# Optimization experiments

Measured on AMD Instinct MI355X. Metric: run time of the kernel, lower is better.

## Reference

```python
import jax, jax.numpy as jnp
import numpy as np

E = 1_000_000   # edges (temporal neighbor facts)
D = 128         # emb_dim
N = 200_000     # nodes carrying hidden state
B = 512         # queries (batch)
R = 240         # num_rel -> rel table has 2R+1 rows
T = 100_000     # tail nodes (scatter output size)


def setup_inputs() -> dict:
    key = jax.random.key(0)
    ks = jax.random.split(key, 14)
    b_col  = jax.random.randint(ks[0], (E,), 0, B)
    n_col  = jax.random.randint(ks[1], (E,), 0, N)
    h_col  = jax.random.randint(ks[2], (E,), 0, N)
    r_col  = jax.random.randint(ks[3], (E,), 0, 2 * R)   # r+1 in [1, 2R]
    t_col  = jax.random.randint(ks[4], (E,), 0, N)
    ts_col = jax.random.randint(ks[5], (E,), 0, 1000)
    facts = jnp.stack([b_col, n_col, h_col, r_col, t_col, ts_col], axis=1)
    s = 1.0 / np.sqrt(D)
    return {
        "hidden":     jax.random.normal(ks[6], (N, D), jnp.float32) * 0.02,
        "rel_table":  jax.random.normal(ks[7], (2 * R + 1, D), jnp.float32) * 0.02,
        "Ws":         jax.random.normal(ks[8], (D, D), jnp.float32) * s,
        "Wr":         jax.random.normal(ks[9], (D, D), jnp.float32) * s,
        "Wqr_w":      jax.random.normal(ks[10], (D, D), jnp.float32) * s,
        "Wqr_b":      jnp.zeros((D,), jnp.float32),
        "wa_w":       jax.random.normal(ks[11], (D, 1), jnp.float32) * s,
        "wa_b":       jnp.zeros((1,), jnp.float32),
        "Wh":         jax.random.normal(ks[12], (D, D), jnp.float32) * s,
        "query_rel":  jax.random.randint(ks[13], (B,), 0, 2 * R),
        "facts":      facts,
        "tail_index": jax.random.randint(jax.random.fold_in(key, 99), (E,), 0, T),
        "tail_nodes": jnp.arange(T),
    }


def reference(hidden, rel_table, Ws, Wr, Wqr_w, Wqr_b, wa_w, wa_b, Wh,
              query_rel, facts, tail_index, tail_nodes):
    b = facts[:, 0]
    n = facts[:, 1]
    r = facts[:, 3]
    h_e = hidden[n]                      # [E, D] gather node hidden
    hr  = rel_table[r + 1]               # [E, D] gather relation emb
    q_r = rel_table[query_rel + 1][b]    # [E, D] per-edge query relation
    # attention MLP: sigmoid(w_alpha(relu(Ws h + Wr r + Wqr q + b)))
    pre = h_e @ Ws + hr @ Wr + (q_r @ Wqr_w + Wqr_b)          # [E, D]
    alpha = jax.nn.sigmoid(jax.nn.relu(pre) @ wa_w + wa_b)    # [E, 1]
    message = alpha * (h_e + hr)                              # [E, D]
    agg = jax.ops.segment_sum(message, tail_index,
                              num_segments=tail_nodes.shape[0])  # [T, D]
    return agg @ Wh                      # act = identity (default)
```

## Files before the change

### kernel.cpp

```cpp
#include <hip/hip_runtime.h>
#include <hip/hip_fp16.h>
#include <math.h>

#define DD 128
#define CAP 64

typedef _Float16 half_t;
typedef __attribute__((ext_vector_type(8))) _Float16 half8;
typedef __attribute__((ext_vector_type(4))) float floatx4;

#define LDW 136

__device__ __forceinline__ __half2 relu2(__half2 x) {
    return __hmul2(x, __hgt2(x, __float2half2_rn(0.f)));
}

template <int CTRL>
__device__ __forceinline__ float dpp_add(float x) {
    int y = __builtin_amdgcn_update_dpp(0, __float_as_int(x), CTRL, 0xf, 0xf, true);
    return x + __int_as_float(y);
}

__global__ void wt4(const float* __restrict__ W0, const float* __restrict__ W1,
                    const float* __restrict__ W2, const float* __restrict__ W3,
                    half_t* __restrict__ T0, half_t* __restrict__ T1,
                    half_t* __restrict__ T2, half_t* __restrict__ T3) {
    const float* W = blockIdx.x == 0 ? W0 : blockIdx.x == 1 ? W1 : blockIdx.x == 2 ? W2 : W3;
    half_t* T      = blockIdx.x == 0 ? T0 : blockIdx.x == 1 ? T1 : blockIdx.x == 2 ? T2 : T3;
    for (int i = threadIdx.x; i < DD * DD; i += blockDim.x) {
        int n = i >> 7, k = i & 127;
        T[i] = (half_t)W[(size_t)k * DD + n];
    }
}

__device__ __forceinline__ void mfma_pass(
    const half_t* As, const half_t* WT, int w, int lane, floatx4 acc[8]) {
    int rowf = lane & 15;
    int kgrp = (lane >> 4) * 8;
#pragma unroll
    for (int t = 0; t < 8; t++) acc[t] = (floatx4){0.f, 0.f, 0.f, 0.f};
    const half_t* ap = As + (w * 16 + rowf) * LDW + kgrp;
    const half_t* bp0 = WT + rowf * LDW + kgrp;
#pragma unroll
    for (int kk = 0; kk < DD; kk += 32) {
        half8 a = *(const half8*)(ap + kk);
#pragma unroll
        for (int t = 0; t < 8; t++) {
            half8 b = *(const half8*)(bp0 + t * 16 * LDW + kk);
            acc[t] = __builtin_amdgcn_mfma_f32_16x16x32_f16(a, b, acc[t], 0, 0, 0);
        }
    }
}

__device__ __forceinline__ void acc_to_lds(const floatx4 acc[8], half_t* OutT,
                                           int w, int lane) {
    int rowf = lane & 15;
    int rbase = w * 16 + (lane >> 4) * 4;
#pragma unroll
    for (int t = 0; t < 8; t++) {
        int col = t * 16 + rowf;
#pragma unroll
        for (int i = 0; i < 4; i++) OutT[(rbase + i) * LDW + col] = (half_t)acc[t][i];
    }
}

__device__ __forceinline__ void lds_to_packed(const half_t* OutT, int tileM, int M,
                                              int tid, __half* Packed, int halfOff) {
    for (int ch = tid; ch < 1024; ch += 256) {
        int row = ch >> 4, off = (ch & 15) * 8;
        int gr = tileM + row;
        if (gr < M) {
            half8 v = *(const half8*)(OutT + row * LDW + off);
            *(uint4*)(Packed + (size_t)gr * 256 + halfOff + off) = *(uint4*)&v;
        }
    }
}

__global__ __launch_bounds__(256) void gemm_pack2(
    const float* __restrict__ table, int M,
    const half_t* __restrict__ WT1_g, const half_t* __restrict__ WT2_g,
    __half* __restrict__ Packed) {
    __shared__ half_t WT[DD * LDW];
    __shared__ half_t As[64 * LDW];
    int tid = threadIdx.x;
    int lane = tid & 63;
    int w = tid >> 6;
    int tileM = blockIdx.x * 64;

    for (int i = tid; i < 2048; i += 256) {
        int row = i >> 5, c4 = i & 31;
        int gr = tileM + row;
        float4 v = make_float4(0.f, 0.f, 0.f, 0.f);
        if (gr < M) v = *(const float4*)(table + (size_t)gr * DD + c4 * 4);
        __half2 h01 = __floats2half2_rn(v.x, v.y);
        __half2 h23 = __floats2half2_rn(v.z, v.w);
        *(uint2*)(As + row * LDW + c4 * 4) = make_uint2(*(unsigned*)&h01, *(unsigned*)&h23);
    }
    for (int i = tid; i < 2048; i += 256) {
        int n = i >> 4, ch = i & 15;
        *(half8*)(WT + n * LDW + ch * 8) = *(const half8*)(WT1_g + n * DD + ch * 8);
    }
    __syncthreads();
    floatx4 acc[8];
    mfma_pass(As, WT, w, lane, acc);
    __syncthreads();
    acc_to_lds(acc, WT, w, lane);
    __syncthreads();
    lds_to_packed(WT, tileM, M, tid, Packed, 0);
    __syncthreads();
    for (int i = tid; i < 2048; i += 256) {
        int n = i >> 4, ch = i & 15;
        *(half8*)(WT + n * LDW + ch * 8) = *(const half8*)(WT2_g + n * DD + ch * 8);
    }
    __syncthreads();
    mfma_pass(As, WT, w, lane, acc);
    __syncthreads();
    acc_to_lds(acc, WT, w, lane);
    __syncthreads();
    lds_to_packed(WT, tileM, M, tid, Packed, 128);
}

__global__ __launch_bounds__(256) void gemm_mfma(
    const float* __restrict__ table, const int* __restrict__ idx, int idxAdd, int M,
    const half_t* __restrict__ WT_g, const float* __restrict__ bias,
    float* __restrict__ OutF, __half* __restrict__ OutH) {
    __shared__ half_t WT[DD * LDW];
    __shared__ half_t As[64 * LDW];
    int tid = threadIdx.x;
    int lane = tid & 63;
    int w = tid >> 6;
    int rowf = lane & 15;

    for (int i = tid; i < 2048; i += 256) {
        int n = i >> 4, ch = i & 15;
        *(half8*)(WT + n * LDW + ch * 8) = *(const half8*)(WT_g + n * DD + ch * 8);
    }
    int tileM = blockIdx.x * 64;
    for (int i = tid; i < 2048; i += 256) {
        int row = i >> 5, c4 = i & 31;
        int gr = tileM + row;
        float4 v = make_float4(0.f, 0.f, 0.f, 0.f);
        if (gr < M) {
            int src = idx ? (idx[gr] + idxAdd) : gr;
            v = *(const float4*)(table + (size_t)src * DD + c4 * 4);
        }
        __half2 h01 = __floats2half2_rn(v.x, v.y);
        __half2 h23 = __floats2half2_rn(v.z, v.w);
        *(uint2*)(As + row * LDW + c4 * 4) = make_uint2(*(unsigned*)&h01, *(unsigned*)&h23);
    }
    __syncthreads();

    floatx4 acc[8];
    mfma_pass(As, WT, w, lane, acc);
    int orow = tileM + w * 16 + (lane >> 4) * 4;
#pragma unroll
    for (int t = 0; t < 8; t++) {
        int col = t * 16 + rowf;
        float bv = bias ? bias[col] : 0.f;
#pragma unroll
        for (int i = 0; i < 4; i++) {
            int gr = orow + i;
            if (gr < M) {
                float o = acc[t][i] + bv;
                if (OutF) OutF[(size_t)gr * DD + col] = o;
                if (OutH) OutH[(size_t)gr * DD + col] = __float2half(o);
            }
        }
    }
}

__global__ __launch_bounds__(256) void alpha_scatter(
    const __half* __restrict__ HB, const __half* __restrict__ RB,
    const __half* __restrict__ QB, const int* __restrict__ facts,
    const int* __restrict__ tail, const float* __restrict__ wa,
    const float* __restrict__ wa_b,
    int* __restrict__ cursor, int2* __restrict__ meta, int E) {
    int tid = threadIdx.x;
    int lane = tid & 63;
    int g = lane >> 4;
    int cl = lane & 15;
    int c = cl * 8;
    int wv = (blockIdx.x * 256 + tid) >> 6;
    int e0 = wv * 16 + g;

    float4 wva = *(const float4*)(wa + c);
    float4 wvb = *(const float4*)(wa + c + 4);
    __half2 w0 = __halves2half2(__float2half(wva.x), __float2half(wva.y));
    __half2 w1 = __halves2half2(__float2half(wva.z), __float2half(wva.w));
    __half2 w2 = __halves2half2(__float2half(wvb.x), __float2half(wvb.y));
    __half2 w3 = __halves2half2(__float2half(wvb.z), __float2half(wvb.w));
    float wb = wa_b[0];

    bool v[4]; int2 bn[4]; int r[4]; int tl[4];
#pragma unroll
    for (int j = 0; j < 4; j++) {
        int f = e0 + j * 4;
        v[j] = f < E;
        int fc = v[j] ? f : 0;
        bn[j] = *(const int2*)(facts + (size_t)fc * 6);
        r[j] = facts[(size_t)fc * 6 + 3];
        tl[j] = tail[fc];
    }

    uint4 h[4], rr[4], q[4];
#pragma unroll
    for (int j = 0; j < 4; j++) {
        h[j]  = *(const uint4*)(HB + (size_t)bn[j].y * 256 + 128 + c);
        rr[j] = *(const uint4*)(RB + (size_t)(r[j] + 1) * 256 + 128 + c);
        q[j]  = *(const uint4*)(QB + (size_t)bn[j].x * DD + c);
    }

    float t[4];
#pragma unroll
    for (int j = 0; j < 4; j++) {
        __half2 p0 = relu2(__hadd2(__hadd2(*(__half2*)&h[j].x, *(__half2*)&rr[j].x),
                                   *(__half2*)&q[j].x));
        __half2 p1 = relu2(__hadd2(__hadd2(*(__half2*)&h[j].y, *(__half2*)&rr[j].y),
                                   *(__half2*)&q[j].y));
        __half2 p2 = relu2(__hadd2(__hadd2(*(__half2*)&h[j].z, *(__half2*)&rr[j].z),
                                   *(__half2*)&q[j].z));
        __half2 p3 = relu2(__hadd2(__hadd2(*(__half2*)&h[j].w, *(__half2*)&rr[j].w),
                                   *(__half2*)&q[j].w));
        __half2 t2 = __hfma2(p1, w1, __hmul2(p0, w0));
        t2 = __hfma2(p2, w2, t2);
        t2 = __hfma2(p3, w3, t2);
        t[j] = __half2float(__low2half(t2)) + __half2float(__high2half(t2));
    }

#pragma unroll
    for (int j = 0; j < 4; j++) {
        t[j] = dpp_add<0x111>(t[j]);
        t[j] = dpp_add<0x112>(t[j]);
        t[j] = dpp_add<0x114>(t[j]);
        t[j] = dpp_add<0x118>(t[j]);
    }

    if (cl == 15) {
#pragma unroll
        for (int j = 0; j < 4; j++) {
            if (v[j]) {
                float a = 1.f / (1.f + __expf(-(t[j] + wb)));
                unsigned ab = (unsigned)__half_as_ushort(__float2half(a));
                int slot = atomicAdd(&cursor[tl[j]], 1);
                if (slot < CAP)
                    meta[(size_t)tl[j] * CAP + slot] =
                        make_int2(bn[j].y, (r[j] + 1) | (int)(ab << 16));
            }
        }
    }
}

__global__ __launch_bounds__(256) void agg_out(
    const __half* __restrict__ HB, const __half* __restrict__ RB,
    const int2* __restrict__ meta, const int* __restrict__ cursor,
    float* __restrict__ out, int T) {
    int w = threadIdx.x >> 6;
    int lane = threadIdx.x & 63;
    int seg = blockIdx.x * 4 + w;
    if (seg >= T) return;
    int cnt = cursor[seg];
    if (cnt > CAP) cnt = CAP;
    const int2* mp = meta + (size_t)seg * CAP;
    int co = lane * 2;
    float ax = 0.f, ay = 0.f;

#define ACC(hu, ru, y_)                                                        \
    {                                                                          \
        __half2 s = __hadd2(*(__half2*)&(hu), *(__half2*)&(ru));               \
        float al =                                                             \
            __half2float(__ushort_as_half((unsigned short)((unsigned)(y_) >> 16))); \
        float2 sf = __half22float2(s);                                         \
        ax = fmaf(al, sf.x, ax);                                               \
        ay = fmaf(al, sf.y, ay);                                               \
    }

    int i = 0;
    for (; i + 7 < cnt; i += 8) {
        int4 ma = *(const int4*)(mp + i);
        int4 mb = *(const int4*)(mp + i + 2);
        int4 mc = *(const int4*)(mp + i + 4);
        int4 md = *(const int4*)(mp + i + 6);
        unsigned h0 = *(const unsigned*)(HB + (size_t)ma.x * 256 + co);
        unsigned r0 = *(const unsigned*)(RB + (size_t)(ma.y & 0xFFFF) * 256 + co);
        unsigned h1 = *(const unsigned*)(HB + (size_t)ma.z * 256 + co);
        unsigned r1 = *(const unsigned*)(RB + (size_t)(ma.w & 0xFFFF) * 256 + co);
        unsigned h2 = *(const unsigned*)(HB + (size_t)mb.x * 256 + co);
        unsigned r2 = *(const unsigned*)(RB + (size_t)(mb.y & 0xFFFF) * 256 + co);
        unsigned h3 = *(const unsigned*)(HB + (size_t)mb.z * 256 + co);
        unsigned r3 = *(const unsigned*)(RB + (size_t)(mb.w & 0xFFFF) * 256 + co);
        unsigned h4 = *(const unsigned*)(HB + (size_t)mc.x * 256 + co);
        unsigned r4 = *(const unsigned*)(RB + (size_t)(mc.y & 0xFFFF) * 256 + co);
        unsigned h5 = *(const unsigned*)(HB + (size_t)mc.z * 256 + co);
        unsigned r5 = *(const unsigned*)(RB + (size_t)(mc.w & 0xFFFF) * 256 + co);
        unsigned h6 = *(const unsigned*)(HB + (size_t)md.x * 256 + co);
        unsigned r6 = *(const unsigned*)(RB + (size_t)(md.y & 0xFFFF) * 256 + co);
        unsigned h7 = *(const unsigned*)(HB + (size_t)md.z * 256 + co);
        unsigned r7 = *(const unsigned*)(RB + (size_t)(md.w & 0xFFFF) * 256 + co);
        ACC(h0, r0, ma.y); ACC(h1, r1, ma.w);
        ACC(h2, r2, mb.y); ACC(h3, r3, mb.w);
        ACC(h4, r4, mc.y); ACC(h5, r5, mc.w);
        ACC(h6, r6, md.y); ACC(h7, r7, md.w);
    }
    for (; i + 3 < cnt; i += 4) {
        int4 ma = *(const int4*)(mp + i);
        int4 mb = *(const int4*)(mp + i + 2);
        unsigned h0 = *(const unsigned*)(HB + (size_t)ma.x * 256 + co);
        unsigned r0 = *(const unsigned*)(RB + (size_t)(ma.y & 0xFFFF) * 256 + co);
        unsigned h1 = *(const unsigned*)(HB + (size_t)ma.z * 256 + co);
        unsigned r1 = *(const unsigned*)(RB + (size_t)(ma.w & 0xFFFF) * 256 + co);
        unsigned h2 = *(const unsigned*)(HB + (size_t)mb.x * 256 + co);
        unsigned r2 = *(const unsigned*)(RB + (size_t)(mb.y & 0xFFFF) * 256 + co);
        unsigned h3 = *(const unsigned*)(HB + (size_t)mb.z * 256 + co);
        unsigned r3 = *(const unsigned*)(RB + (size_t)(mb.w & 0xFFFF) * 256 + co);
        ACC(h0, r0, ma.y); ACC(h1, r1, ma.w);
        ACC(h2, r2, mb.y); ACC(h3, r3, mb.w);
    }
    for (; i < cnt; i++) {
        int2 m = mp[i];
        unsigned hu = *(const unsigned*)(HB + (size_t)m.x * 256 + co);
        unsigned ru = *(const unsigned*)(RB + (size_t)(m.y & 0xFFFF) * 256 + co);
        ACC(hu, ru, m.y);
    }
#undef ACC

    *(float2*)(out + (size_t)seg * DD + co) = make_float2(ax, ay);
}

extern "C" void kernel_launch(void* const* d_in, const int* in_sizes, int n_in,
                              void* d_out, int out_size, void* d_ws, size_t ws_size,
                              hipStream_t stream) {
    const float* hidden    = (const float*)d_in[0];
    const float* rel_table = (const float*)d_in[1];
    const float* Ws        = (const float*)d_in[2];
    const float* Wr        = (const float*)d_in[3];
    const float* Wqr_w     = (const float*)d_in[4];
    const float* Wqr_b     = (const float*)d_in[5];
    const float* wa_w      = (const float*)d_in[6];
    const float* wa_b      = (const float*)d_in[7];
    const float* Wh        = (const float*)d_in[8];
    const int* query_rel   = (const int*)d_in[9];
    const int* facts       = (const int*)d_in[10];
    const int* tail_index  = (const int*)d_in[11];

    int N     = in_sizes[0] / DD;
    int Rrows = in_sizes[1] / DD;
    int B     = in_sizes[9];
    int E     = in_sizes[11];
    int T     = in_sizes[12];

    char* ws = (char*)d_ws;
    size_t off = 0;
    auto alloc = [&](size_t bytes) -> void* {
        void* p = ws + off;
        off += (bytes + 255) & ~(size_t)255;
        return p;
    };
    __half* HB  = (__half*)alloc((size_t)N * 256 * 2);
    __half* RB  = (__half*)alloc((size_t)Rrows * 256 * 2);
    __half* QB  = (__half*)alloc((size_t)B * DD * 2);
    int* cursor = (int*)alloc((size_t)T * 4);
    int2* meta  = (int2*)alloc((size_t)T * CAP * 8);
    half_t* WsT  = (half_t*)alloc((size_t)DD * DD * 2);
    half_t* WrT  = (half_t*)alloc((size_t)DD * DD * 2);
    half_t* WqrT = (half_t*)alloc((size_t)DD * DD * 2);
    half_t* WhT  = (half_t*)alloc((size_t)DD * DD * 2);

    (void)hipMemsetAsync(cursor, 0, (size_t)T * 4, stream);

    wt4<<<4, 256, 0, stream>>>(Ws, Wr, Wqr_w, Wh, WsT, WrT, WqrT, WhT);

    gemm_pack2<<<(N + 63) / 64, 256, 0, stream>>>(hidden, N, WhT, WsT, HB);
    gemm_pack2<<<(Rrows + 63) / 64, 256, 0, stream>>>(rel_table, Rrows, WhT, WrT, RB);
    gemm_mfma<<<(B + 63) / 64, 256, 0, stream>>>(rel_table, query_rel, 1, B,
                                                 WqrT, Wqr_b, nullptr, QB);

    alpha_scatter<<<(E + 63) / 64, 256, 0, stream>>>(HB, RB, QB, facts, tail_index,
                                                     wa_w, wa_b, cursor, meta, E);

    agg_out<<<(T + 3) / 4, 256, 0, stream>>>(HB, RB, meta, cursor,
                                             (float*)d_out, T);
}
```

Before: 448.2 us.

## Pre-swizzle weights into MFMA fragment order and stream A fragments from global

Weights are converted once into a layout that matches the MFMA B-fragment order, so each lane reads its fragment with one contiguous vector load. The node/relation projection kernel now uses 1024-thread blocks, each wave owning 16-row tiles. It loads A fragments straight from global memory into registers and writes results directly to global instead of going through LDS with several barriers. The cost is more LDS per block (two weight matrices), uncoalesced scalar half stores to the packed output, and lower occupancy from the larger block.

```diff
diff --git a/kernel.cpp b/kernel.cpp
--- a/kernel.cpp
+++ b/kernel.cpp
@@ -21,103 +21,89 @@
     return x + __int_as_float(y);
 }
 
-__global__ void wt4(const float* __restrict__ W0, const float* __restrict__ W1,
-                    const float* __restrict__ W2, const float* __restrict__ W3,
-                    half_t* __restrict__ T0, half_t* __restrict__ T1,
-                    half_t* __restrict__ T2, half_t* __restrict__ T3) {
-    const float* W = blockIdx.x == 0 ? W0 : blockIdx.x == 1 ? W1 : blockIdx.x == 2 ? W2 : W3;
-    half_t* T      = blockIdx.x == 0 ? T0 : blockIdx.x == 1 ? T1 : blockIdx.x == 2 ? T2 : T3;
-    for (int i = threadIdx.x; i < DD * DD; i += blockDim.x) {
-        int n = i >> 7, k = i & 127;
-        T[i] = (half_t)W[(size_t)k * DD + n];
-    }
-}
-
-__device__ __forceinline__ void mfma_pass(
-    const half_t* As, const half_t* WT, int w, int lane, floatx4 acc[8]) {
-    int rowf = lane & 15;
-    int kgrp = (lane >> 4) * 8;
-#pragma unroll
-    for (int t = 0; t < 8; t++) acc[t] = (floatx4){0.f, 0.f, 0.f, 0.f};
-    const half_t* ap = As + (w * 16 + rowf) * LDW + kgrp;
-    const half_t* bp0 = WT + rowf * LDW + kgrp;
-#pragma unroll
-    for (int kk = 0; kk < DD; kk += 32) {
-        half8 a = *(const half8*)(ap + kk);
-#pragma unroll
-        for (int t = 0; t < 8; t++) {
-            half8 b = *(const half8*)(bp0 + t * 16 * LDW + kk);
-            acc[t] = __builtin_amdgcn_mfma_f32_16x16x32_f16(a, b, acc[t], 0, 0, 0);
-        }
-    }
-}
-
-__device__ __forceinline__ void acc_to_lds(const floatx4 acc[8], half_t* OutT,
-                                           int w, int lane) {
-    int rowf = lane & 15;
-    int rbase = w * 16 + (lane >> 4) * 4;
-#pragma unroll
-    for (int t = 0; t < 8; t++) {
-        int col = t * 16 + rowf;
-#pragma unroll
-        for (int i = 0; i < 4; i++) OutT[(rbase + i) * LDW + col] = (half_t)acc[t][i];
-    }
-}
-
-__device__ __forceinline__ void lds_to_packed(const half_t* OutT, int tileM, int M,
-                                              int tid, __half* Packed, int halfOff) {
-    for (int ch = tid; ch < 1024; ch += 256) {
-        int row = ch >> 4, off = (ch & 15) * 8;
-        int gr = tileM + row;
-        if (gr < M) {
-            half8 v = *(const half8*)(OutT + row * LDW + off);
-            *(uint4*)(Packed + (size_t)gr * 256 + halfOff + off) = *(uint4*)&v;
-        }
-    }
-}
-
-__global__ __launch_bounds__(256) void gemm_pack2(
+__global__ void wprep(const float* __restrict__ Wh, const float* __restrict__ Ws,
+                      const float* __restrict__ Wr, const float* __restrict__ Wqr,
+                      half_t* __restrict__ WhF, half_t* __restrict__ WsF,
+                      half_t* __restrict__ WrF, half_t* __restrict__ WqrT) {
+    int m = blockIdx.x;
+    if (m < 3) {
+        const float* W = m == 0 ? Wh : m == 1 ? Ws : Wr;
+        half_t* F      = m == 0 ? WhF : m == 1 ? WsF : WrF;
+        for (int idx = threadIdx.x; idx < 2048; idx += blockDim.x) {
+            int lane = idx & 63, kkI = (idx >> 6) & 3, t = idx >> 8;
+            int n = t * 16 + (lane & 15);
+            int k0 = kkI * 32 + (lane >> 4) * 8;
+            half_t tmp[8];
+#pragma unroll
+            for (int j = 0; j < 8; j++) tmp[j] = (half_t)W[(size_t)(k0 + j) * DD + n];
+            *(half8*)(F + (size_t)idx * 8) = *(half8*)tmp;
+        }
+    } else {
+        for (int i = threadIdx.x; i < DD * DD; i += blockDim.x) {
+            int n = i >> 7, k = i & 127;
+            WqrT[i] = (half_t)Wqr[(size_t)k * DD + n];
+        }
+    }
+}
+
+__global__ __launch_bounds__(1024) void gemm_pack2v(
     const float* __restrict__ table, int M,
-    const half_t* __restrict__ WT1_g, const half_t* __restrict__ WT2_g,
+    const half_t* __restrict__ W1F, const half_t* __restrict__ W2F,
     __half* __restrict__ Packed) {
-    __shared__ half_t WT[DD * LDW];
-    __shared__ half_t As[64 * LDW];
+    __shared__ half_t WF[2 * 2048 * 8];
     int tid = threadIdx.x;
-    int lane = tid & 63;
-    int w = tid >> 6;
-    int tileM = blockIdx.x * 64;
-
-    for (int i = tid; i < 2048; i += 256) {
-        int row = i >> 5, c4 = i & 31;
-        int gr = tileM + row;
-        float4 v = make_float4(0.f, 0.f, 0.f, 0.f);
-        if (gr < M) v = *(const float4*)(table + (size_t)gr * DD + c4 * 4);
-        __half2 h01 = __floats2half2_rn(v.x, v.y);
-        __half2 h23 = __floats2half2_rn(v.z, v.w);
-        *(uint2*)(As + row * LDW + c4 * 4) = make_uint2(*(unsigned*)&h01, *(unsigned*)&h23);
-    }
-    for (int i = tid; i < 2048; i += 256) {
-        int n = i >> 4, ch = i & 15;
-        *(half8*)(WT + n * LDW + ch * 8) = *(const half8*)(WT1_g + n * DD + ch * 8);
+    for (int i = tid; i < 4096; i += 1024) {
+        const half_t* src = (i < 2048) ? (W1F + (size_t)i * 8)
+                                       : (W2F + (size_t)(i - 2048) * 8);
+        *(half8*)(WF + (size_t)i * 8) = *(const half8*)src;
     }
     __syncthreads();
-    floatx4 acc[8];
-    mfma_pass(As, WT, w, lane, acc);
-    __syncthreads();
-    acc_to_lds(acc, WT, w, lane);
-    __syncthreads();
-    lds_to_packed(WT, tileM, M, tid, Packed, 0);
-    __syncthreads();
-    for (int i = tid; i < 2048; i += 256) {
-        int n = i >> 4, ch = i & 15;
-        *(half8*)(WT + n * LDW + ch * 8) = *(const half8*)(WT2_g + n * DD + ch * 8);
-    }
-    __syncthreads();
-    mfma_pass(As, WT, w, lane, acc);
-    __syncthreads();
-    acc_to_lds(acc, WT, w, lane);
-    __syncthreads();
-    lds_to_packed(WT, tileM, M, tid, Packed, 128);
+
+    int w = tid >> 6, lane = tid & 63;
+    int nt = (M + 15) >> 4;
+    for (int tile = blockIdx.x * 16 + w; tile < nt; tile += gridDim.x * 16) {
+        int row = tile * 16 + (lane & 15);
+        int rs = row < M ? row : M - 1;
+        int k0 = (lane >> 4) * 8;
+        half8 afr[4];
+#pragma unroll
+        for (int kkI = 0; kkI < 4; kkI++) {
+            const float* p = table + (size_t)rs * DD + kkI * 32 + k0;
+            float4 va = *(const float4*)p;
+            float4 vb = *(const float4*)(p + 4);
+            half8 a;
+            a[0] = (half_t)va.x; a[1] = (half_t)va.y;
+            a[2] = (half_t)va.z; a[3] = (half_t)va.w;
+            a[4] = (half_t)vb.x; a[5] = (half_t)vb.y;
+            a[6] = (half_t)vb.z; a[7] = (half_t)vb.w;
+            afr[kkI] = a;
+        }
+#pragma unroll
+        for (int m = 0; m < 2; m++) {
+            floatx4 acc[8];
+#pragma unroll
+            for (int t = 0; t < 8; t++) acc[t] = (floatx4){0.f, 0.f, 0.f, 0.f};
+#pragma unroll
+            for (int t = 0; t < 8; t++)
+#pragma unroll
+                for (int kkI = 0; kkI < 4; kkI++) {
+                    half8 b = *(const half8*)(WF +
+                        (((size_t)(m * 8 + t) * 4 + kkI) * 64 + lane) * 8);
+                    acc[t] = __builtin_amdgcn_mfma_f32_16x16x32_f16(afr[kkI], b, acc[t], 0, 0, 0);
+                }
+            int rbase = tile * 16 + (lane >> 4) * 4;
+#pragma unroll
+            for (int t = 0; t < 8; t++) {
+                int col = t * 16 + (lane & 15);
+#pragma unroll
+                for (int i2 = 0; i2 < 4; i2++) {
+                    int gr = rbase + i2;
+                    if (gr < M)
+                        Packed[(size_t)gr * 256 + m * 128 + col] = __float2half(acc[t][i2]);
+                }
+            }
+        }
+    }
 }
 
 __global__ __launch_bounds__(256) void gemm_mfma(
@@ -130,6 +116,7 @@
     int lane = tid & 63;
     int w = tid >> 6;
     int rowf = lane & 15;
+    int kgrp = (lane >> 4) * 8;
 
     for (int i = tid; i < 2048; i += 256) {
         int n = i >> 4, ch = i & 15;
@@ -151,7 +138,19 @@
     __syncthreads();
 
     floatx4 acc[8];
-    mfma_pass(As, WT, w, lane, acc);
+#pragma unroll
+    for (int t = 0; t < 8; t++) acc[t] = (floatx4){0.f, 0.f, 0.f, 0.f};
+    const half_t* ap = As + (w * 16 + rowf) * LDW + kgrp;
+    const half_t* bp0 = WT + rowf * LDW + kgrp;
+#pragma unroll
+    for (int kk = 0; kk < DD; kk += 32) {
+        half8 a = *(const half8*)(ap + kk);
+#pragma unroll
+        for (int t = 0; t < 8; t++) {
+            half8 b = *(const half8*)(bp0 + t * 16 * LDW + kk);
+            acc[t] = __builtin_amdgcn_mfma_f32_16x16x32_f16(a, b, acc[t], 0, 0, 0);
+        }
+    }
     int orow = tileM + w * 16 + (lane >> 4) * 4;
 #pragma unroll
     for (int t = 0; t < 8; t++) {
@@ -360,17 +359,19 @@
     __half* QB  = (__half*)alloc((size_t)B * DD * 2);
     int* cursor = (int*)alloc((size_t)T * 4);
     int2* meta  = (int2*)alloc((size_t)T * CAP * 8);
-    half_t* WsT  = (half_t*)alloc((size_t)DD * DD * 2);
-    half_t* WrT  = (half_t*)alloc((size_t)DD * DD * 2);
+    half_t* WhF  = (half_t*)alloc((size_t)DD * DD * 2);
+    half_t* WsF  = (half_t*)alloc((size_t)DD * DD * 2);
+    half_t* WrF  = (half_t*)alloc((size_t)DD * DD * 2);
     half_t* WqrT = (half_t*)alloc((size_t)DD * DD * 2);
-    half_t* WhT  = (half_t*)alloc((size_t)DD * DD * 2);
 
     (void)hipMemsetAsync(cursor, 0, (size_t)T * 4, stream);
 
-    wt4<<<4, 256, 0, stream>>>(Ws, Wr, Wqr_w, Wh, WsT, WrT, WqrT, WhT);
-
-    gemm_pack2<<<(N + 63) / 64, 256, 0, stream>>>(hidden, N, WhT, WsT, HB);
-    gemm_pack2<<<(Rrows + 63) / 64, 256, 0, stream>>>(rel_table, Rrows, WhT, WrT, RB);
+    wprep<<<4, 256, 0, stream>>>(Wh, Ws, Wr, Wqr_w, WhF, WsF, WrF, WqrT);
+
+    int ntN = (N + 15) >> 4;
+    gemm_pack2v<<<(ntN + 15) / 16, 1024, 0, stream>>>(hidden, N, WhF, WsF, HB);
+    int ntR = (Rrows + 15) >> 4;
+    gemm_pack2v<<<(ntR + 15) / 16, 1024, 0, stream>>>(rel_table, Rrows, WhF, WrF, RB);
     gemm_mfma<<<(B + 63) / 64, 256, 0, stream>>>(rel_table, query_rel, 1, B,
                                                  WqrT, Wqr_b, nullptr, QB);
 
```

Result: slower. 726.8 us (+62.2%).
